# Performance work log

Measured on AMD Instinct MI355X. Metric: run time of the kernel, lower is better.

Reference implementation:

```python
import jax, jax.numpy as jnp
from jax import lax
import numpy as np
import math

ALPHA = 1000.0
BETA = 100.0
K = 24
INIT_DIM = 64
STAGES = 4
NUM_POINTS = 2048
B = 16
EPS = 1e-5


def embedding_spe(x, out_dim):
    # x: [..., in_dim] -> [..., out_dim] sinusoidal embedding
    in_dim = x.shape[-1]
    feat_dim = math.ceil(out_dim / (in_dim * 2))
    dim_embed = jnp.asarray(ALPHA ** (np.arange(feat_dim) / feat_dim), x.dtype)
    feat_num = feat_dim * 2 * in_dim
    out_idx = np.linspace(0, feat_num - 1, out_dim).astype(np.int64)
    div = BETA * x[..., None] / dim_embed            # [..., in_dim, feat_dim]
    pe = jnp.stack([jnp.sin(div), jnp.cos(div)], -1)  # [..., in_dim, feat_dim, 2]
    pe = pe.reshape(x.shape[:-1] + (feat_num,))       # order matches torch cat(flatten(stack))
    return pe[..., out_idx]


def fps_single(xyz, npoint):
    # xyz: [N,3] -> indices [npoint] (deterministic start at index 0)
    n = xyz.shape[0]

    def body(carry, _):
        dist, farthest = carry
        centroid = xyz[farthest]
        d = jnp.sum((xyz - centroid) ** 2, -1)
        dist = jnp.minimum(dist, d)
        nxt = jnp.argmax(dist).astype(jnp.int32)
        return (dist, nxt), farthest

    init = (jnp.full((n,), 1e10, xyz.dtype), jnp.array(0, jnp.int32))
    _, idx = lax.scan(body, init, None, length=npoint)
    return idx


def knn(k, xyz, new_xyz):
    # xyz [B,N,3], new_xyz [B,S,3] -> [B,S,k] indices of k nearest points
    d = (jnp.sum(new_xyz ** 2, -1, keepdims=True)
         + jnp.sum(xyz ** 2, -1)[:, None, :]
         - 2.0 * jnp.einsum('bsc,bnc->bsn', new_xyz, xyz))
    _, idx = lax.top_k(-d, k)
    return idx


def gather(pts, idx):
    # pts [B,N,C], idx [B,...] -> [B,...,C]
    b = pts.shape[0]
    bi = jnp.arange(b).reshape((b,) + (1,) * (idx.ndim - 1))
    return pts[bi, idx]


def stage(xyz, feat, npoint, out_dim, gamma, beta_p):
    fps_idx = jax.vmap(lambda p: fps_single(p, npoint))(lax.stop_gradient(xyz))
    xyz_s = gather(xyz, fps_idx)    # [B,S,3]
    feat_s = gather(feat, fps_idx)  # [B,S,C]
    idx_knn = knn(K, lax.stop_gradient(xyz), lax.stop_gradient(xyz_s))  # [B,S,K]
    xyz_knn = gather(xyz, idx_knn)    # [B,S,K,3]
    feat_knn = gather(feat, idx_knn)  # [B,S,K,C]
    # normalize by global (unbiased) std, like torch.std over whole tensor
    xyz_c = xyz_knn - xyz_s[:, :, None, :]
    xyz_knn = xyz_c / (jnp.std(xyz_c, ddof=1) + 1e-05)
    feat_c = feat_knn - feat_s[:, :, None, :]
    feat_knn = feat_c / (jnp.std(feat_c, ddof=1) + 1e-05)
    bsz, s, k, c = feat_knn.shape
    feat_knn = jnp.concatenate(
        [feat_knn, jnp.broadcast_to(feat_s[:, :, None, :], (bsz, s, k, c))], -1)  # [B,S,K,2C]
    # SPE aggregation
    pe = embedding_spe(xyz_knn, out_dim)
    w = (feat_knn + pe) * pe
    # neighbor pooling: max + mean over K
    agg = jnp.max(w, -2) + jnp.mean(w, -2)  # [B,S,out_dim]
    # BatchNorm1d (training-mode batch stats, biased var) + exact GELU
    mean = jnp.mean(agg, axis=(0, 1))
    var = jnp.var(agg, axis=(0, 1))
    y = gamma * (agg - mean) / jnp.sqrt(var + EPS) + beta_p
    return xyz_s, jax.nn.gelu(y, approximate=False)


def setup_inputs() -> dict:
    key = jax.random.key(0)
    ks = jax.random.split(key, 2)
    inp = {'xyz': jax.random.normal(ks[0], (B, NUM_POINTS, 3), jnp.float32)}
    dim = INIT_DIM
    for i in range(STAGES):
        dim *= 2
        inp[f'gamma{i}'] = jnp.ones((dim,), jnp.float32)
        inp[f'beta{i}'] = jnp.zeros((dim,), jnp.float32)
    return inp


def reference(xyz, gamma0, beta0, gamma1, beta1, gamma2, beta2, gamma3, beta3):
    gammas = [gamma0, gamma1, gamma2, gamma3]
    betas = [beta0, beta1, beta2, beta3]
    feat = embedding_spe(xyz, INIT_DIM)
    npoint, dim = NUM_POINTS, INIT_DIM
    for i in range(STAGES):
        dim *= 2
        npoint //= 2
        xyz, feat = stage(xyz, feat, npoint, dim, gammas[i], betas[i])
    return jnp.max(feat, -2) + jnp.mean(feat, -2)  # [B, 1024]
```

## Files before the change

### kernel.cpp

```cpp
#include <hip/hip_runtime.h>
#include <math.h>

#pragma clang fp contract(off)

static constexpr int BATCH = 16;
static constexpr int NPTS0 = 2048;
static constexpr int KNN = 24;

static constexpr size_t OFF_STATS = 0;
static constexpr size_t OFF_BN    = 256;
static constexpr size_t OFF_DE    = 32768;
static constexpr size_t OFF_MAP   = 36864;
static constexpr size_t OFF_XYZ1  = 49152;
static constexpr size_t OFF_XYZ2  = OFF_XYZ1 + (size_t)16*1024*3*4;
static constexpr size_t OFF_XYZ3  = OFF_XYZ2 + (size_t)16*512*3*4;
static constexpr size_t OFF_XYZ4  = OFF_XYZ3 + (size_t)16*256*3*4;
static constexpr size_t OFF_FPS0  = OFF_XYZ4 + (size_t)16*128*3*4;
static constexpr size_t OFF_FPS1  = OFF_FPS0 + (size_t)16*1024*4;
static constexpr size_t OFF_FPS2  = OFF_FPS1 + (size_t)16*512*4;
static constexpr size_t OFF_FPS3  = OFF_FPS2 + (size_t)16*256*4;
static constexpr size_t OFF_KNN   = OFF_FPS3 + (size_t)16*128*4;
static constexpr size_t OFF_FEATA = OFF_KNN + (size_t)16*1024*24*4;
static constexpr size_t OFF_FEATB = OFF_FEATA + (size_t)16*2048*64*4;
static constexpr size_t OFF_FEATS = OFF_FEATB + (size_t)16*2048*64*4;
static constexpr size_t OFF_AGG   = OFF_FEATS + (size_t)16*1024*64*4;
static constexpr size_t WS_NEED   = OFF_AGG + (size_t)16*1024*128*4;

__device__ inline uint64_t kmax64(uint64_t a, uint64_t b) { return a > b ? a : b; }

template <int CTRL>
__device__ inline uint64_t dpp_shift64(uint64_t k) {
  int hi = (int)(unsigned)(k >> 32), lo = (int)(unsigned)k;
  int oh = __builtin_amdgcn_update_dpp(hi, hi, CTRL, 0xF, 0xF, false);
  int ol = __builtin_amdgcn_update_dpp(lo, lo, CTRL, 0xF, 0xF, false);
  return ((uint64_t)(unsigned)oh << 32) | (unsigned)ol;
}
__device__ inline uint64_t wave_reduce_max64(uint64_t k) {
  k = kmax64(k, dpp_shift64<0x111>(k));
  k = kmax64(k, dpp_shift64<0x112>(k));
  k = kmax64(k, dpp_shift64<0x114>(k));
  k = kmax64(k, dpp_shift64<0x118>(k));
  k = kmax64(k, dpp_shift64<0x142>(k));
  k = kmax64(k, dpp_shift64<0x143>(k));
  return k;
}

__device__ inline unsigned sortable_f32(float f) {
  unsigned b = __float_as_uint(f);
  unsigned m = (unsigned)((int)b >> 31) | 0x80000000u;
  return b ^ m;
}

__device__ inline unsigned med3u(unsigned a, unsigned b, unsigned c) {
  unsigned r;
  asm("v_med3_u32 %0, %1, %2, %3" : "=v"(r) : "v"(a), "v"(b), "v"(c));
  return r;
}

__device__ inline void ins24(unsigned kk[KNN], unsigned v) {
#pragma unroll
  for (int e = KNN - 1; e >= 1; --e) kk[e] = med3u(kk[e - 1], kk[e], v);
  kk[0] = kk[0] < v ? kk[0] : v;
}

__global__ void init_tables(float* __restrict__ de, int* __restrict__ mp) {
  const int outs[5] = {64, 128, 256, 512, 1024};
  const int fds[5]  = {11, 22, 43, 86, 171};
  const int deo[5]  = {0, 11, 33, 76, 162};
  const int mpo[5]  = {0, 64, 192, 448, 960};
  const int tid = threadIdx.x;
  for (int c = 0; c < 5; ++c) {
    const int fd = fds[c], out = outs[c];
    for (int j = tid; j < fd; j += blockDim.x)
      de[deo[c] + j] = (float)pow(1000.0, (double)j / (double)fd);
    const double step = (double)(6 * fd - 1) / (double)(out - 1);
    for (int f = tid; f < out; f += blockDim.x)
      mp[mpo[c] + f] = (int)(step * (double)f);
  }
}

__global__ __launch_bounds__(256) void embed_init(const float* __restrict__ xyz,
                                                  float* __restrict__ feat,
                                                  const float* __restrict__ de,
                                                  const int* __restrict__ mp) {
  int g = blockIdx.x * blockDim.x + threadIdx.x;
  if (g >= BATCH * NPTS0 * 64) return;
  int c = g & 63;
  int bn = g >> 6;
  int m = mp[c];
  int sc = m & 1;
  int a = m >> 1;
  int ci = a / 11;
  int j = a - ci * 11;
  float x = xyz[bn * 3 + ci];
  float ang = (100.0f * x) / de[j];
  feat[g] = sc ? cosf(ang) : sinf(ang);
}

template <int PTS>
__device__ void fps_stage(const float* lds_cur, float* lds_next,
                          int* __restrict__ fps_idx, float* __restrict__ xyz_next,
                          uint64_t* red) {
  const int S = PTS * 128;
  const int tid = threadIdx.x;
  __syncthreads();
  float px[PTS], py[PTS], pz[PTS], dist[PTS];
  const unsigned nl = ~(unsigned)tid;
#pragma unroll
  for (int p = 0; p < PTS; ++p) {
    int gi = tid + p * 256;
    px[p] = lds_cur[3 * gi];
    py[p] = lds_cur[3 * gi + 1];
    pz[p] = lds_cur[3 * gi + 2];
    dist[p] = 1e10f;
  }
  unsigned sel = 0;
  if (tid == 0) {
    fps_idx[0] = 0;
    float a = lds_cur[0], b = lds_cur[1], c = lds_cur[2];
    xyz_next[0] = a; xyz_next[1] = b; xyz_next[2] = c;
    lds_next[0] = a; lds_next[1] = b; lds_next[2] = c;
  }
  for (int t = 1; t < S; ++t) {
    float cx = lds_cur[3 * sel], cy = lds_cur[3 * sel + 1], cz = lds_cur[3 * sel + 2];
    uint64_t kb = 0;
#pragma unroll
    for (int p = 0; p < PTS; ++p) {
      float dx = px[p] - cx, dy = py[p] - cy, dz = pz[p] - cz;
      float dd = dx * dx + dy * dy;
      dd = dd + dz * dz;
      float nd = fminf(dist[p], dd);
      dist[p] = nd;
      uint64_t key = ((uint64_t)__float_as_uint(nd) << 32) | (unsigned)(nl - (unsigned)(p * 256));
      kb = kmax64(kb, key);
    }
    kb = wave_reduce_max64(kb);
    if ((tid & 63) == 63) red[(t & 1) * 4 + (tid >> 6)] = kb;
    __syncthreads();
    uint64_t k0 = red[(t & 1) * 4 + 0], k1 = red[(t & 1) * 4 + 1];
    uint64_t k2 = red[(t & 1) * 4 + 2], k3 = red[(t & 1) * 4 + 3];
    uint64_t km = kmax64(kmax64(k0, k1), kmax64(k2, k3));
    sel = ~(unsigned)km;
    if (tid == 0) {
      fps_idx[t] = (int)sel;
      float a = lds_cur[3 * sel], b = lds_cur[3 * sel + 1], c = lds_cur[3 * sel + 2];
      xyz_next[3 * t] = a; xyz_next[3 * t + 1] = b; xyz_next[3 * t + 2] = c;
      lds_next[3 * t] = a; lds_next[3 * t + 1] = b; lds_next[3 * t + 2] = c;
    }
  }
}

__global__ __launch_bounds__(256) void fps_all(const float* __restrict__ xyz0,
                                               float* __restrict__ xyz1, float* __restrict__ xyz2,
                                               float* __restrict__ xyz3, float* __restrict__ xyz4,
                                               int* __restrict__ i0, int* __restrict__ i1,
                                               int* __restrict__ i2, int* __restrict__ i3) {
  __shared__ float lds[3 * (2048 + 1024 + 512 + 256 + 128)];
  __shared__ uint64_t red[8];
  const int b = blockIdx.x;
  float* l0 = lds;
  float* l1 = l0 + 3 * 2048;
  float* l2 = l1 + 3 * 1024;
  float* l3 = l2 + 3 * 512;
  float* l4 = l3 + 3 * 256;
  for (int t = threadIdx.x; t < 3 * 2048; t += 256) l0[t] = xyz0[(size_t)b * 3 * 2048 + t];
  fps_stage<8>(l0, l1, i0 + b * 1024, xyz1 + (size_t)b * 1024 * 3, red);
  fps_stage<4>(l1, l2, i1 + b * 512, xyz2 + (size_t)b * 512 * 3, red);
  fps_stage<2>(l2, l3, i2 + b * 256, xyz3 + (size_t)b * 256 * 3, red);
  fps_stage<1>(l3, l4, i3 + b * 128, xyz4 + (size_t)b * 128 * 3, red);
}

static constexpr int MGS = 29;
__global__ __launch_bounds__(256) void knn_tau(const float* __restrict__ db_xyz,
                                               const float* __restrict__ q_xyz,
                                               unsigned* __restrict__ tau,
                                               int Np, int S) {
  extern __shared__ float smem[];
  float4* db = (float4*)smem;
  unsigned* mg = (unsigned*)(db + Np);
  const int tid = threadIdx.x, lane = tid & 63, wv = tid >> 6;
  const int bpb = S >> 6;
  const int b = blockIdx.x / bpb;
  const int qbase = (blockIdx.x % bpb) * 64;
  for (int j = tid; j < Np; j += 256) {
    float x = db_xyz[((size_t)b * Np + j) * 3 + 0];
    float y = db_xyz[((size_t)b * Np + j) * 3 + 1];
    float z = db_xyz[((size_t)b * Np + j) * 3 + 2];
    float pn = x * x + y * y;
    pn = pn + z * z;
    db[j] = make_float4(x, y, z, pn);
  }
  __syncthreads();
  const int s = qbase + lane;
  float qx = q_xyz[((size_t)b * S + s) * 3 + 0];
  float qy = q_xyz[((size_t)b * S + s) * 3 + 1];
  float qz = q_xyz[((size_t)b * S + s) * 3 + 2];
  float qn = qx * qx + qy * qy;
  qn = qn + qz * qz;
  unsigned kk[KNN];
#pragma unroll
  for (int e = 0; e < KNN; ++e) kk[e] = 0xFFFFFFFFu;
  const int cpw = Np >> 2;
  const int beg = wv * cpw, end = beg + cpw;
  for (int j0 = beg; j0 < end; j0 += 8) {
    float4 p[8];
#pragma unroll
    for (int u = 0; u < 8; ++u) p[u] = db[j0 + u];
#pragma unroll
    for (int u = 0; u < 8; ++u) {
      float dot = fmaf(qz, p[u].z, fmaf(qy, p[u].y, qx * p[u].x));
      float d = (qn + p[u].w) - 2.0f * dot;
      unsigned su = sortable_f32(d);
      if (__any(su < kk[KNN - 1])) ins24(kk, su);
    }
  }
  unsigned* myrow = mg + (wv * 64 + lane) * MGS;
#pragma unroll
  for (int e = 0; e < KNN; ++e) myrow[e] = kk[e];
  __syncthreads();
  if (wv == 0) {
    for (int w = 1; w < 4; ++w) {
      const unsigned* orow = mg + (w * 64 + lane) * MGS;
#pragma unroll
      for (int e = 0; e < KNN; ++e) {
        unsigned v = orow[e];
        if (__any(v < kk[KNN - 1])) ins24(kk, v);
      }
    }
    tau[(size_t)b * S + s] = kk[KNN - 1];
  }
}

__global__ __launch_bounds__(256) void knn_collect(const float* __restrict__ db_xyz,
                                                   const float* __restrict__ q_xyz,
                                                   const unsigned* __restrict__ tau,
                                                   int* __restrict__ out_idx,
                                                   int Np, int S) {
  __shared__ uint64_t bufA[4][24];
  __shared__ uint64_t bufB[4][24];
  const int lane = threadIdx.x & 63, wv = threadIdx.x >> 6;
  const int qi = blockIdx.x * 4 + wv;
  const int b = qi / S, s = qi % S;
  float qx = q_xyz[((size_t)b * S + s) * 3 + 0];
  float qy = q_xyz[((size_t)b * S + s) * 3 + 1];
  float qz = q_xyz[((size_t)b * S + s) * 3 + 2];
  float qn = qx * qx + qy * qy;
  qn = qn + qz * qz;
  const unsigned tt = tau[qi];
  int cntA = 0, cntB = 0;
  const unsigned long long lmlt = (1ull << lane) - 1;
  const int iters = Np >> 6;
  for (int it = 0; it < iters; ++it) {
    int j = it * 64 + lane;
    float x = db_xyz[((size_t)b * Np + j) * 3 + 0];
    float y = db_xyz[((size_t)b * Np + j) * 3 + 1];
    float z = db_xyz[((size_t)b * Np + j) * 3 + 2];
    float pn = x * x + y * y;
    pn = pn + z * z;
    float dot = fmaf(qz, z, fmaf(qy, y, qx * x));
    float d = (qn + pn) - 2.0f * dot;
    unsigned su = sortable_f32(d);
    unsigned long long mlt = __ballot(su < tt);
    unsigned long long meq = __ballot(su == tt);
    if (mlt) {
      int pos = cntA + __popcll(mlt & lmlt);
      if (su < tt && pos < 24) bufA[wv][pos] = ((uint64_t)su << 32) | (unsigned)j;
      cntA += __popcll(mlt);
    }
    if (meq) {
      int pos = cntB + __popcll(meq & lmlt);
      if (su == tt && pos < 24) bufB[wv][pos] = ((uint64_t)su << 32) | (unsigned)j;
      cntB += __popcll(meq);
    }
  }
  uint64_t v = (lane < cntA) ? bufA[wv][lane] : ~0ull;
#pragma unroll
  for (int k = 2; k <= 64; k <<= 1) {
#pragma unroll
    for (int m = k >> 1; m > 0; m >>= 1) {
      uint64_t o = __shfl_xor(v, m);
      bool takemin = (((lane & k) == 0) == ((lane & m) == 0));
      uint64_t mn = v < o ? v : o;
      uint64_t mx = v < o ? o : v;
      v = takemin ? mn : mx;
    }
  }
  if (lane < KNN) {
    uint64_t key = (lane < cntA) ? v : bufB[wv][lane - cntA];
    out_idx[(size_t)qi * KNN + lane] = (int)(unsigned)key;
  }
}

__global__ __launch_bounds__(256) void gather_feat_s(const float* __restrict__ feat,
                                                     const int* __restrict__ fidx,
                                                     float* __restrict__ out, int Np, int S, int C) {
  int g = blockIdx.x * blockDim.x + threadIdx.x;
  if (g >= BATCH * S * C) return;
  int c = g % C;
  int bs = g / C;
  int s = bs % S;
  int b = bs / S;
  int src = fidx[b * S + s];
  out[g] = feat[((size_t)b * Np + src) * C + c];
}

__global__ __launch_bounds__(256) void center_reduce(const float* __restrict__ xyz,
                                                     const float* __restrict__ xyz_s,
                                                     const float* __restrict__ feat,
                                                     const float* __restrict__ feat_s,
                                                     const int* __restrict__ kidx,
                                                     double* __restrict__ sums,
                                                     int Np, int S, int C) {
  int g = blockIdx.x * blockDim.x + threadIdx.x;
  int total = BATCH * S * KNN;
  double sx = 0, sxx = 0, sf = 0, sff = 0;
  if (g < total) {
    int bs = g / KNN;
    int s = bs % S;
    int b = bs / S;
    int j = kidx[g];
    const float* pc = xyz + ((size_t)b * Np + j) * 3;
    const float* qc = xyz_s + ((size_t)b * S + s) * 3;
    for (int c = 0; c < 3; ++c) {
      float v = pc[c] - qc[c];
      sx += (double)v;
      sxx += (double)v * (double)v;
    }
    const float4* fr = (const float4*)(feat + ((size_t)b * Np + j) * C);
    const float4* fs = (const float4*)(feat_s + ((size_t)b * S + s) * C);
    for (int c = 0; c < C / 4; ++c) {
      float4 a = fr[c], bq = fs[c];
      float v0 = a.x - bq.x, v1 = a.y - bq.y, v2 = a.z - bq.z, v3 = a.w - bq.w;
      sf += (double)v0 + (double)v1 + (double)v2 + (double)v3;
      sff += (double)v0 * v0 + (double)v1 * v1 + (double)v2 * v2 + (double)v3 * v3;
    }
  }
#pragma unroll
  for (int m = 1; m < 64; m <<= 1) {
    sx += __shfl_xor(sx, m);
    sxx += __shfl_xor(sxx, m);
    sf += __shfl_xor(sf, m);
    sff += __shfl_xor(sff, m);
  }
  __shared__ double part[4][4];
  int wv = threadIdx.x >> 6;
  if ((threadIdx.x & 63) == 0) { part[wv][0] = sx; part[wv][1] = sxx; part[wv][2] = sf; part[wv][3] = sff; }
  __syncthreads();
  if (threadIdx.x == 0) {
    double a = 0, b2 = 0, c2 = 0, d2 = 0;
    for (int w = 0; w < 4; ++w) { a += part[w][0]; b2 += part[w][1]; c2 += part[w][2]; d2 += part[w][3]; }
    atomicAdd(&sums[0], a);
    atomicAdd(&sums[1], b2);
    atomicAdd(&sums[2], c2);
    atomicAdd(&sums[3], d2);
  }
}

template <int CH>
__global__ __launch_bounds__(256) void agg_kernel(const float* __restrict__ xyz,
                                                  const float* __restrict__ xyz_s,
                                                  const float* __restrict__ feat,
                                                  const float* __restrict__ feat_s,
                                                  const int* __restrict__ kidx,
                                                  const double* __restrict__ csums,
                                                  const float* __restrict__ de,
                                                  const int* __restrict__ mp,
                                                  float* __restrict__ agg,
                                                  int Np, int S, int C, int fd,
                                                  double nx_d, double nf_d) {
  const int lane = threadIdx.x & 63;
  const int wv = threadIdx.x >> 6;
  const int q = blockIdx.x * 4 + wv;
  const int s = q % S;
  const int b = q / S;
  double sxd = csums[0], sxxd = csums[1], sfd = csums[2], sffd = csums[3];
  float stdx = sqrtf((float)((sxxd - sxd * sxd / nx_d) / (nx_d - 1.0)));
  float stdf = sqrtf((float)((sffd - sfd * sfd / nf_d) / (nf_d - 1.0)));
  float invx = 1.0f / (stdx + 1e-5f);
  float invf = 1.0f / (stdf + 1e-5f);
  float cx = xyz_s[((size_t)b * S + s) * 3 + 0];
  float cy = xyz_s[((size_t)b * S + s) * 3 + 1];
  float cz = xyz_s[((size_t)b * S + s) * 3 + 2];
  const float* fsrow = feat_s + ((size_t)b * S + s) * C;
  int ci[CH];
  float dev[CH], fsv[CH];
  bool issin[CH], fh[CH];
#pragma unroll
  for (int ch = 0; ch < CH; ++ch) {
    int f = ch * 64 + lane;
    int m = mp[f];
    issin[ch] = (m & 1) == 0;
    int a = m >> 1;
    int cc = a / fd;
    ci[ch] = cc;
    dev[ch] = de[a - cc * fd];
    fh[ch] = f < C;
    fsv[ch] = fh[ch] ? fsrow[f] : fsrow[f - C];
  }
  float wmax[CH], wsum[CH];
#pragma unroll
  for (int ch = 0; ch < CH; ++ch) { wmax[ch] = -3.4e38f; wsum[ch] = 0.f; }
  const int* krow = kidx + ((size_t)b * S + s) * KNN;
  for (int k = 0; k < KNN; ++k) {
    int j = krow[k];
    const float* pr = xyz + ((size_t)b * Np + j) * 3;
    float n0 = (pr[0] - cx) * invx;
    float n1 = (pr[1] - cy) * invx;
    float n2 = (pr[2] - cz) * invx;
    const float* fr = feat + ((size_t)b * Np + j) * C;
#pragma unroll
    for (int ch = 0; ch < CH; ++ch) {
      float xv = (ci[ch] == 0) ? n0 : ((ci[ch] == 1) ? n1 : n2);
      float ang = (100.0f * xv) / dev[ch];
      float sv, cv;
      sincosf(ang, &sv, &cv);
      float pef = issin[ch] ? sv : cv;
      int f = ch * 64 + lane;
      float val = fh[ch] ? (fr[f] - fsv[ch]) * invf : fsv[ch];
      float w = (val + pef) * pef;
      wmax[ch] = fmaxf(wmax[ch], w);
      wsum[ch] += w;
    }
  }
  float* arow = agg + (size_t)q * (CH * 64);
#pragma unroll
  for (int ch = 0; ch < CH; ++ch) {
    int f = ch * 64 + lane;
    arow[f] = wmax[ch] + wsum[ch] / (float)KNN;
  }
}

__global__ __launch_bounds__(256) void bn_reduce(const float* __restrict__ agg,
                                                 double* __restrict__ bns,
                                                 int R, int D) {
  int r0 = blockIdx.x * 64;
  for (int c = threadIdx.x; c < D; c += 256) {
    double s = 0, ss = 0;
    for (int r = 0; r < 64; ++r) {
      float v = agg[(size_t)(r0 + r) * D + c];
      s += (double)v;
      ss += (double)v * (double)v;
    }
    atomicAdd(&bns[c], s);
    atomicAdd(&bns[D + c], ss);
  }
}

__global__ __launch_bounds__(256) void bn_apply(const float* __restrict__ agg,
                                                const double* __restrict__ bns,
                                                const float* __restrict__ gamma,
                                                const float* __restrict__ beta,
                                                float* __restrict__ outf, int R, int D) {
  int g = blockIdx.x * blockDim.x + threadIdx.x;
  if (g >= R * D) return;
  int c = g % D;
  double n = (double)R;
  double mu = bns[c] / n;
  double var = bns[D + c] / n - mu * mu;
  float mean = (float)mu;
  float rstd = 1.0f / sqrtf((float)var + 1e-5f);
  float x = (agg[g] - mean) * rstd;
  float y = gamma[c] * x + beta[c];
  float e = erff(y * 0.70710678118654752440f);
  outf[g] = 0.5f * y * (1.0f + e);
}

__global__ __launch_bounds__(256) void final_kernel(const float* __restrict__ feat,
                                                    float* __restrict__ out) {
  int g = blockIdx.x * blockDim.x + threadIdx.x;
  if (g >= BATCH * 1024) return;
  int f = g % 1024;
  int b = g / 1024;
  const float* base = feat + (size_t)b * 128 * 1024 + f;
  float mx = -3.4e38f;
  float sm = 0.f;
  for (int s = 0; s < 128; ++s) {
    float v = base[(size_t)s * 1024];
    mx = fmaxf(mx, v);
    sm += v;
  }
  out[g] = mx + sm / 128.0f;
}

extern "C" void kernel_launch(void* const* d_in, const int* in_sizes, int n_in,
                              void* d_out, int out_size, void* d_ws, size_t ws_size,
                              hipStream_t stream) {
  (void)in_sizes; (void)n_in; (void)out_size;
  if (ws_size < WS_NEED) return;
  const float* xyz = (const float*)d_in[0];
  const float* gam[4] = {(const float*)d_in[1], (const float*)d_in[3], (const float*)d_in[5], (const float*)d_in[7]};
  const float* bet[4] = {(const float*)d_in[2], (const float*)d_in[4], (const float*)d_in[6], (const float*)d_in[8]};
  char* ws = (char*)d_ws;
  double* stats = (double*)(ws + OFF_STATS);
  double* bns = (double*)(ws + OFF_BN);
  float* de = (float*)(ws + OFF_DE);
  int* mp = (int*)(ws + OFF_MAP);
  float* xyz1 = (float*)(ws + OFF_XYZ1);
  float* xyz2 = (float*)(ws + OFF_XYZ2);
  float* xyz3 = (float*)(ws + OFF_XYZ3);
  float* xyz4 = (float*)(ws + OFF_XYZ4);
  int* fpsI[4] = {(int*)(ws + OFF_FPS0), (int*)(ws + OFF_FPS1), (int*)(ws + OFF_FPS2), (int*)(ws + OFF_FPS3)};
  int* kidx = (int*)(ws + OFF_KNN);
  float* feata = (float*)(ws + OFF_FEATA);
  float* featb = (float*)(ws + OFF_FEATB);
  float* feats = (float*)(ws + OFF_FEATS);
  unsigned* tau = (unsigned*)(ws + OFF_FEATS);
  float* agg = (float*)(ws + OFF_AGG);

  hipMemsetAsync(ws, 0, 32768, stream);
  init_tables<<<1, 256, 0, stream>>>(de, mp);
  fps_all<<<16, 256, 0, stream>>>(xyz, xyz1, xyz2, xyz3, xyz4, fpsI[0], fpsI[1], fpsI[2], fpsI[3]);
  embed_init<<<(BATCH * NPTS0 * 64) / 256, 256, 0, stream>>>(xyz, feata, de, mp);

  const int Ns[4] = {2048, 1024, 512, 256};
  const int Cs[4] = {64, 128, 256, 512};
  const int fdv[4] = {22, 43, 86, 171};
  const int deo[4] = {11, 33, 76, 162};
  const int mpo[4] = {64, 192, 448, 960};
  const float* xin[5] = {xyz, xyz1, xyz2, xyz3, xyz4};
  float* fcur = feata;
  float* fnext = featb;
  int bnoff = 0;
  for (int i = 0; i < 4; ++i) {
    const int Np = Ns[i], S = Np / 2, C = Cs[i], D = 2 * C;
    size_t tau_lds = (size_t)Np * 16 + (size_t)4 * 64 * MGS * 4;
    knn_tau<<<16 * (S / 64), 256, tau_lds, stream>>>(xin[i], xin[i + 1], tau, Np, S);
    knn_collect<<<(BATCH * S) / 4, 256, 0, stream>>>(xin[i], xin[i + 1], tau, kidx, Np, S);
    gather_feat_s<<<(BATCH * S * C) / 256, 256, 0, stream>>>(fcur, fpsI[i], feats, Np, S, C);
    const int tuples = BATCH * S * KNN;
    center_reduce<<<(tuples + 255) / 256, 256, 0, stream>>>(xin[i], xin[i + 1], fcur, feats, kidx,
                                                            stats + 4 * i, Np, S, C);
    double nx = (double)tuples * 3.0;
    double nf = (double)tuples * (double)C;
    dim3 ag((BATCH * S) / 4);
    switch (D / 64) {
      case 2:
        agg_kernel<2><<<ag, 256, 0, stream>>>(xin[i], xin[i + 1], fcur, feats, kidx, stats + 4 * i,
                                              de + deo[i], mp + mpo[i], agg, Np, S, C, fdv[i], nx, nf);
        break;
      case 4:
        agg_kernel<4><<<ag, 256, 0, stream>>>(xin[i], xin[i + 1], fcur, feats, kidx, stats + 4 * i,
                                              de + deo[i], mp + mpo[i], agg, Np, S, C, fdv[i], nx, nf);
        break;
      case 8:
        agg_kernel<8><<<ag, 256, 0, stream>>>(xin[i], xin[i + 1], fcur, feats, kidx, stats + 4 * i,
                                              de + deo[i], mp + mpo[i], agg, Np, S, C, fdv[i], nx, nf);
        break;
      default:
        agg_kernel<16><<<ag, 256, 0, stream>>>(xin[i], xin[i + 1], fcur, feats, kidx, stats + 4 * i,
                                               de + deo[i], mp + mpo[i], agg, Np, S, C, fdv[i], nx, nf);
        break;
    }
    const int R = BATCH * S;
    bn_reduce<<<R / 64, 256, 0, stream>>>(agg, bns + bnoff, R, D);
    bn_apply<<<(R * D) / 256, 256, 0, stream>>>(agg, bns + bnoff, gam[i], bet[i], fnext, R, D);
    bnoff += 2 * D;
    float* t = fcur; fcur = fnext; fnext = t;
  }
  final_kernel<<<(BATCH * 1024) / 256, 256, 0, stream>>>(fcur, (float*)d_out);
}
```

Baseline: 1.753 ms.

## Fuse embed into FPS launch, drop feat_s gather, fuse final BN with pooling

Several launch-level fusions. The memset moves into init_tables, and the embedding kernel is folded into the FPS launch as extra blocks so it runs alongside the long serial FPS blocks. The gather_feat_s kernel is removed, so center_reduce and agg_kernel read centroid features through the FPS index. The last stage's bn_apply is fused with the final max+mean pooling. These changes cut kernel launches and intermediate buffer traffic, at the cost of indirect reads in the consumers.

```diff
diff --git a/kernel.cpp b/kernel.cpp
--- a/kernel.cpp
+++ b/kernel.cpp
@@ -22,8 +22,8 @@
 static constexpr size_t OFF_KNN   = OFF_FPS3 + (size_t)16*128*4;
 static constexpr size_t OFF_FEATA = OFF_KNN + (size_t)16*1024*24*4;
 static constexpr size_t OFF_FEATB = OFF_FEATA + (size_t)16*2048*64*4;
-static constexpr size_t OFF_FEATS = OFF_FEATB + (size_t)16*2048*64*4;
-static constexpr size_t OFF_AGG   = OFF_FEATS + (size_t)16*1024*64*4;
+static constexpr size_t OFF_TAU   = OFF_FEATB + (size_t)16*2048*64*4;
+static constexpr size_t OFF_AGG   = OFF_TAU + (size_t)16*1024*64*4;
 static constexpr size_t WS_NEED   = OFF_AGG + (size_t)16*1024*128*4;
 
 __device__ inline uint64_t kmax64(uint64_t a, uint64_t b) { return a > b ? a : b; }
@@ -63,12 +63,14 @@
   kk[0] = kk[0] < v ? kk[0] : v;
 }
 
-__global__ void init_tables(float* __restrict__ de, int* __restrict__ mp) {
+__global__ void init_tables(float* __restrict__ de, int* __restrict__ mp,
+                            double* __restrict__ zero_region) {
   const int outs[5] = {64, 128, 256, 512, 1024};
   const int fds[5]  = {11, 22, 43, 86, 171};
   const int deo[5]  = {0, 11, 33, 76, 162};
   const int mpo[5]  = {0, 64, 192, 448, 960};
   const int tid = threadIdx.x;
+  for (int u = tid; u < 4096; u += 256) zero_region[u] = 0.0;
   for (int c = 0; c < 5; ++c) {
     const int fd = fds[c], out = outs[c];
     for (int j = tid; j < fd; j += blockDim.x)
@@ -77,24 +79,6 @@
     for (int f = tid; f < out; f += blockDim.x)
       mp[mpo[c] + f] = (int)(step * (double)f);
   }
-}
-
-__global__ __launch_bounds__(256) void embed_init(const float* __restrict__ xyz,
-                                                  float* __restrict__ feat,
-                                                  const float* __restrict__ de,
-                                                  const int* __restrict__ mp) {
-  int g = blockIdx.x * blockDim.x + threadIdx.x;
-  if (g >= BATCH * NPTS0 * 64) return;
-  int c = g & 63;
-  int bn = g >> 6;
-  int m = mp[c];
-  int sc = m & 1;
-  int a = m >> 1;
-  int ci = a / 11;
-  int j = a - ci * 11;
-  float x = xyz[bn * 3 + ci];
-  float ang = (100.0f * x) / de[j];
-  feat[g] = sc ? cosf(ang) : sinf(ang);
 }
 
 template <int PTS>
@@ -150,13 +134,30 @@
   }
 }
 
-__global__ __launch_bounds__(256) void fps_all(const float* __restrict__ xyz0,
-                                               float* __restrict__ xyz1, float* __restrict__ xyz2,
-                                               float* __restrict__ xyz3, float* __restrict__ xyz4,
-                                               int* __restrict__ i0, int* __restrict__ i1,
-                                               int* __restrict__ i2, int* __restrict__ i3) {
+__global__ __launch_bounds__(256) void fps_embed(const float* __restrict__ xyz0,
+                                                 float* __restrict__ xyz1, float* __restrict__ xyz2,
+                                                 float* __restrict__ xyz3, float* __restrict__ xyz4,
+                                                 int* __restrict__ i0, int* __restrict__ i1,
+                                                 int* __restrict__ i2, int* __restrict__ i3,
+                                                 float* __restrict__ feat,
+                                                 const float* __restrict__ de,
+                                                 const int* __restrict__ mp) {
   __shared__ float lds[3 * (2048 + 1024 + 512 + 256 + 128)];
   __shared__ uint64_t red[8];
+  if (blockIdx.x >= 16) {
+    int g = (blockIdx.x - 16) * 256 + threadIdx.x;
+    int c = g & 63;
+    int bn = g >> 6;
+    int m = mp[c];
+    int sc = m & 1;
+    int a = m >> 1;
+    int ci = a / 11;
+    int j = a - ci * 11;
+    float x = xyz0[bn * 3 + ci];
+    float ang = (100.0f * x) / de[j];
+    feat[g] = sc ? cosf(ang) : sinf(ang);
+    return;
+  }
   const int b = blockIdx.x;
   float* l0 = lds;
   float* l1 = l0 + 3 * 2048;
@@ -291,23 +292,10 @@
   }
 }
 
-__global__ __launch_bounds__(256) void gather_feat_s(const float* __restrict__ feat,
-                                                     const int* __restrict__ fidx,
-                                                     float* __restrict__ out, int Np, int S, int C) {
-  int g = blockIdx.x * blockDim.x + threadIdx.x;
-  if (g >= BATCH * S * C) return;
-  int c = g % C;
-  int bs = g / C;
-  int s = bs % S;
-  int b = bs / S;
-  int src = fidx[b * S + s];
-  out[g] = feat[((size_t)b * Np + src) * C + c];
-}
-
 __global__ __launch_bounds__(256) void center_reduce(const float* __restrict__ xyz,
                                                      const float* __restrict__ xyz_s,
                                                      const float* __restrict__ feat,
-                                                     const float* __restrict__ feat_s,
+                                                     const int* __restrict__ fidx,
                                                      const int* __restrict__ kidx,
                                                      double* __restrict__ sums,
                                                      int Np, int S, int C) {
@@ -319,6 +307,7 @@
     int s = bs % S;
     int b = bs / S;
     int j = kidx[g];
+    int src = fidx[bs];
     const float* pc = xyz + ((size_t)b * Np + j) * 3;
     const float* qc = xyz_s + ((size_t)b * S + s) * 3;
     for (int c = 0; c < 3; ++c) {
@@ -327,7 +316,7 @@
       sxx += (double)v * (double)v;
     }
     const float4* fr = (const float4*)(feat + ((size_t)b * Np + j) * C);
-    const float4* fs = (const float4*)(feat_s + ((size_t)b * S + s) * C);
+    const float4* fs = (const float4*)(feat + ((size_t)b * Np + src) * C);
     for (int c = 0; c < C / 4; ++c) {
       float4 a = fr[c], bq = fs[c];
       float v0 = a.x - bq.x, v1 = a.y - bq.y, v2 = a.z - bq.z, v3 = a.w - bq.w;
@@ -360,7 +349,7 @@
 __global__ __launch_bounds__(256) void agg_kernel(const float* __restrict__ xyz,
                                                   const float* __restrict__ xyz_s,
                                                   const float* __restrict__ feat,
-                                                  const float* __restrict__ feat_s,
+                                                  const int* __restrict__ fidx,
                                                   const int* __restrict__ kidx,
                                                   const double* __restrict__ csums,
                                                   const float* __restrict__ de,
@@ -381,7 +370,7 @@
   float cx = xyz_s[((size_t)b * S + s) * 3 + 0];
   float cy = xyz_s[((size_t)b * S + s) * 3 + 1];
   float cz = xyz_s[((size_t)b * S + s) * 3 + 2];
-  const float* fsrow = feat_s + ((size_t)b * S + s) * C;
+  const float* fsrow = feat + ((size_t)b * Np + fidx[b * S + s]) * C;
   int ci[CH];
   float dev[CH], fsv[CH];
   bool issin[CH], fh[CH];
@@ -465,17 +454,30 @@
   outf[g] = 0.5f * y * (1.0f + e);
 }
 
-__global__ __launch_bounds__(256) void final_kernel(const float* __restrict__ feat,
-                                                    float* __restrict__ out) {
+__global__ __launch_bounds__(256) void bn_apply_final(const float* __restrict__ agg,
+                                                      const double* __restrict__ bns,
+                                                      const float* __restrict__ gamma,
+                                                      const float* __restrict__ beta,
+                                                      float* __restrict__ out) {
+  const int D = 1024;
   int g = blockIdx.x * blockDim.x + threadIdx.x;
-  if (g >= BATCH * 1024) return;
-  int f = g % 1024;
-  int b = g / 1024;
-  const float* base = feat + (size_t)b * 128 * 1024 + f;
+  if (g >= BATCH * D) return;
+  int f = g % D;
+  int b = g / D;
+  double n = 2048.0;
+  double mu = bns[f] / n;
+  double var = bns[D + f] / n - mu * mu;
+  float mean = (float)mu;
+  float rstd = 1.0f / sqrtf((float)var + 1e-5f);
+  float gm = gamma[f], bt = beta[f];
+  const float* base = agg + (size_t)b * 128 * D + f;
   float mx = -3.4e38f;
   float sm = 0.f;
   for (int s = 0; s < 128; ++s) {
-    float v = base[(size_t)s * 1024];
+    float x = (base[(size_t)s * D] - mean) * rstd;
+    float y = gm * x + bt;
+    float e = erff(y * 0.70710678118654752440f);
+    float v = 0.5f * y * (1.0f + e);
     mx = fmaxf(mx, v);
     sm += v;
   }
@@ -503,14 +505,12 @@
   int* kidx = (int*)(ws + OFF_KNN);
   float* feata = (float*)(ws + OFF_FEATA);
   float* featb = (float*)(ws + OFF_FEATB);
-  float* feats = (float*)(ws + OFF_FEATS);
-  unsigned* tau = (unsigned*)(ws + OFF_FEATS);
+  unsigned* tau = (unsigned*)(ws + OFF_TAU);
   float* agg = (float*)(ws + OFF_AGG);
 
-  hipMemsetAsync(ws, 0, 32768, stream);
-  init_tables<<<1, 256, 0, stream>>>(de, mp);
-  fps_all<<<16, 256, 0, stream>>>(xyz, xyz1, xyz2, xyz3, xyz4, fpsI[0], fpsI[1], fpsI[2], fpsI[3]);
-  embed_init<<<(BATCH * NPTS0 * 64) / 256, 256, 0, stream>>>(xyz, feata, de, mp);
+  init_tables<<<1, 256, 0, stream>>>(de, mp, (double*)ws);
+  fps_embed<<<16 + 8192, 256, 0, stream>>>(xyz, xyz1, xyz2, xyz3, xyz4,
+                                           fpsI[0], fpsI[1], fpsI[2], fpsI[3], feata, de, mp);
 
   const int Ns[4] = {2048, 1024, 512, 256};
   const int Cs[4] = {64, 128, 256, 512};
@@ -526,36 +526,39 @@
     size_t tau_lds = (size_t)Np * 16 + (size_t)4 * 64 * MGS * 4;
     knn_tau<<<16 * (S / 64), 256, tau_lds, stream>>>(xin[i], xin[i + 1], tau, Np, S);
     knn_collect<<<(BATCH * S) / 4, 256, 0, stream>>>(xin[i], xin[i + 1], tau, kidx, Np, S);
-    gather_feat_s<<<(BATCH * S * C) / 256, 256, 0, stream>>>(fcur, fpsI[i], feats, Np, S, C);
     const int tuples = BATCH * S * KNN;
-    center_reduce<<<(tuples + 255) / 256, 256, 0, stream>>>(xin[i], xin[i + 1], fcur, feats, kidx,
+    center_reduce<<<(tuples + 255) / 256, 256, 0, stream>>>(xin[i], xin[i + 1], fcur, fpsI[i], kidx,
                                                             stats + 4 * i, Np, S, C);
     double nx = (double)tuples * 3.0;
     double nf = (double)tuples * (double)C;
     dim3 ag((BATCH * S) / 4);
     switch (D / 64) {
       case 2:
-        agg_kernel<2><<<ag, 256, 0, stream>>>(xin[i], xin[i + 1], fcur, feats, kidx, stats + 4 * i,
+        agg_kernel<2><<<ag, 256, 0, stream>>>(xin[i], xin[i + 1], fcur, fpsI[i], kidx, stats + 4 * i,
                                               de + deo[i], mp + mpo[i], agg, Np, S, C, fdv[i], nx, nf);
         break;
       case 4:
-        agg_kernel<4><<<ag, 256, 0, stream>>>(xin[i], xin[i + 1], fcur, feats, kidx, stats + 4 * i,
+        agg_kernel<4><<<ag, 256, 0, stream>>>(xin[i], xin[i + 1], fcur, fpsI[i], kidx, stats + 4 * i,
                                               de + deo[i], mp + mpo[i], agg, Np, S, C, fdv[i], nx, nf);
         break;
       case 8:
-        agg_kernel<8><<<ag, 256, 0, stream>>>(xin[i], xin[i + 1], fcur, feats, kidx, stats + 4 * i,
+        agg_kernel<8><<<ag, 256, 0, stream>>>(xin[i], xin[i + 1], fcur, fpsI[i], kidx, stats + 4 * i,
                                               de + deo[i], mp + mpo[i], agg, Np, S, C, fdv[i], nx, nf);
         break;
       default:
-        agg_kernel<16><<<ag, 256, 0, stream>>>(xin[i], xin[i + 1], fcur, feats, kidx, stats + 4 * i,
+        agg_kernel<16><<<ag, 256, 0, stream>>>(xin[i], xin[i + 1], fcur, fpsI[i], kidx, stats + 4 * i,
                                                de + deo[i], mp + mpo[i], agg, Np, S, C, fdv[i], nx, nf);
         break;
     }
     const int R = BATCH * S;
     bn_reduce<<<R / 64, 256, 0, stream>>>(agg, bns + bnoff, R, D);
-    bn_apply<<<(R * D) / 256, 256, 0, stream>>>(agg, bns + bnoff, gam[i], bet[i], fnext, R, D);
+    if (i < 3) {
+      bn_apply<<<(R * D) / 256, 256, 0, stream>>>(agg, bns + bnoff, gam[i], bet[i], fnext, R, D);
+    } else {
+      bn_apply_final<<<(BATCH * 1024) / 256, 256, 0, stream>>>(agg, bns + bnoff, gam[3], bet[3],
+                                                               (float*)d_out);
+    }
     bnoff += 2 * D;
     float* t = fcur; fcur = fnext; fnext = t;
   }
-  final_kernel<<<(BATCH * 1024) / 256, 256, 0, stream>>>(fcur, (float*)d_out);
-}
+}
```

After: 1.779 ms. About the same (+1.4%).
